# Kernel tuning notes

Measured on AMD Instinct MI355X. Metric: run time of the kernel, lower is better.

Reference implementation:

```python
import jax, jax.numpy as jnp
import numpy as np

N, E = 50000, 800000
HID, EDGE_DIM, HEADS = 128, 16, 4
C = HID // HEADS  # 32
NEG_SLOPE = 0.2  # GATv2Conv default negative_slope


def setup_inputs() -> dict:
    key = jax.random.key(0)
    ks = jax.random.split(key, 16)
    def glorot(k, shape):
        fan_in = shape[0]
        return jax.random.normal(k, shape, jnp.float32) / np.sqrt(fan_in)
    return {
        "x": jax.random.normal(ks[0], (N, HID), jnp.float32),
        "edge_index": jax.random.randint(ks[1], (2, E), 0, N, jnp.int64 if jax.config.jax_enable_x64 else jnp.int32),
        "edge_attr": jax.random.normal(ks[2], (E, EDGE_DIM), jnp.float32),
        # GATv2Conv params (lin_l, lin_r with bias; lin_edge bias-free; att; final bias)
        "Wl": glorot(ks[3], (HID, HID)),
        "bl": jnp.zeros((HID,), jnp.float32),
        "Wr": glorot(ks[4], (HID, HID)),
        "br": jnp.zeros((HID,), jnp.float32),
        "We": glorot(ks[5], (EDGE_DIM, HID)),
        "att": glorot(ks[6], (HEADS, C)),
        "bias_gat": jnp.zeros((HID,), jnp.float32),
        # RMSNorm weights
        "w_norm1": jnp.ones((HID,), jnp.float32),
        "w_norm2": jnp.ones((HID,), jnp.float32),
        # FFN params
        "ffn_w1": glorot(ks[7], (HID, 4 * HID)),
        "ffn_b1": jnp.zeros((4 * HID,), jnp.float32),
        "ffn_w2": glorot(ks[8], (4 * HID, HID)),
        "ffn_b2": jnp.zeros((HID,), jnp.float32),
    }


def rmsnorm(x, w):
    # torch.nn.RMSNorm with eps=None -> eps = finfo(dtype).eps
    eps = jnp.finfo(x.dtype).eps
    ms = jnp.mean(x * x, axis=-1, keepdims=True)
    return x * jax.lax.rsqrt(ms + eps) * w


def gatv2_conv(x, edge_index, edge_attr, Wl, bl, Wr, br, We, att, bias_gat):
    n = x.shape[0]
    h, c = att.shape
    xl = (x @ Wl + bl).reshape(n, h, c)   # source-side transform (x_j)
    xr = (x @ Wr + br).reshape(n, h, c)   # target-side transform (x_i)
    src, dst = edge_index[0], edge_index[1]
    e = (edge_attr @ We).reshape(-1, h, c)
    m = xl[src] + xr[dst] + e                       # [E, H, C] per-edge message pre-activation
    s = jnp.where(m > 0, m, NEG_SLOPE * m)          # LeakyReLU(0.2)
    logits = jnp.einsum('ehc,hc->eh', s, att)       # [E, H]
    # scatter-softmax over edges grouped by target node
    lmax = jax.ops.segment_max(logits, dst, num_segments=n)
    ex = jnp.exp(logits - lmax[dst])
    den = jax.ops.segment_sum(ex, dst, num_segments=n)
    alpha = ex / (den[dst] + 1e-16)                 # PyG softmax denominator guard
    out = jax.ops.segment_sum(alpha[..., None] * xl[src], dst, num_segments=n)
    return out.reshape(n, h * c) + bias_gat


def reference(x, edge_index, edge_attr, Wl, bl, Wr, br, We, att, bias_gat,
              w_norm1, w_norm2, ffn_w1, ffn_b1, ffn_w2, ffn_b2):
    x_attn = gatv2_conv(x, edge_index, edge_attr, Wl, bl, Wr, br, We, att, bias_gat)
    h = rmsnorm(x + x_attn, w_norm1)
    f = jax.nn.gelu(h @ ffn_w1 + ffn_b1, approximate=False) @ ffn_w2 + ffn_b2
    return rmsnorm(h + f, w_norm2)
```

## Files before the change

kernel.cpp:

```cpp
#include <hip/hip_runtime.h>

#define NN 50000
#define EE 800000

typedef unsigned short u16;

#define OFF_GAT  0u
#define OFF_XLB  6400000u
#define OFF_XRB  9600000u
#define OFF_SE   12800000u
#define OFF_CNT  14400000u
#define OFF_OFS  14450000u
#define OFF_H    6400000u
#define OFF_WLRT 14500004u
#define OFF_W1T  14516388u
#define OFF_W2T  14549156u

#define RMS_EPS 1.1920928955078125e-7f

typedef float f32x4v __attribute__((ext_vector_type(4)));
typedef short s16x8 __attribute__((ext_vector_type(8)));

__device__ __forceinline__ f32x4v mfma16(s16x8 a, s16x8 b, f32x4v c) {
  return __builtin_amdgcn_mfma_f32_16x16x32_bf16(a, b, c, 0, 0, 0);
}
__device__ __forceinline__ u16 f2b(float f) {
  unsigned int u = __float_as_uint(f);
  unsigned int r = (u + 0x7fffu + ((u >> 16) & 1u)) >> 16;
  return (u16)r;
}
__device__ __forceinline__ float b2f(u16 u) {
  union { float f; unsigned int i; } x; x.i = ((unsigned int)u) << 16; return x.f;
}
__device__ __forceinline__ s16x8 ld_bf16x8_f32(const float* __restrict__ p) {
  float4 v0 = *(const float4*)p;
  float4 v1 = *(const float4*)(p + 4);
  s16x8 r;
  r[0] = (short)f2b(v0.x); r[1] = (short)f2b(v0.y);
  r[2] = (short)f2b(v0.z); r[3] = (short)f2b(v0.w);
  r[4] = (short)f2b(v1.x); r[5] = (short)f2b(v1.y);
  r[6] = (short)f2b(v1.z); r[7] = (short)f2b(v1.w);
  return r;
}
__device__ __forceinline__ float readlane_f32(float v, int lane) {
  return __int_as_float(__builtin_amdgcn_readlane(__float_as_int(v), lane));
}
__device__ __forceinline__ int readlane_i32(int v, int lane) {
  return __builtin_amdgcn_readlane(v, lane);
}

__global__ __launch_bounds__(256) void k_prep(const float* __restrict__ Wl, const float* __restrict__ Wr,
    const float* __restrict__ W1, const float* __restrict__ W2,
    int* __restrict__ cnt, u16* __restrict__ wlrt, u16* __restrict__ w1t, u16* __restrict__ w2t)
{
  int i = blockIdx.x * 256 + threadIdx.x;
  if (i < NN) cnt[i] = 0;
  if (i < 32768) {
    int n = i >> 7, k = i & 127;
    float v = (n < 128) ? Wl[k * 128 + n] : Wr[k * 128 + (n - 128)];
    wlrt[i] = f2b(v);
  }
  {
    int n = i >> 7, k = i & 127;
    w1t[i] = f2b(W1[k * 512 + n]);
  }
  {
    int n = i >> 9, k = i & 511;
    w2t[i] = f2b(W2[k * 128 + n]);
  }
}

__global__ __launch_bounds__(256) void k_hist(const int* __restrict__ ei, int* __restrict__ cnt) {
  int e = blockIdx.x * 256 + threadIdx.x;
  if (e < EE) atomicAdd(&cnt[ei[EE + e]], 1);
}

__global__ __launch_bounds__(1024) void k_scan(const int* __restrict__ cnt,
    int* __restrict__ offs, int* __restrict__ pos)
{
  __shared__ int wsum[16];
  __shared__ int carry_s;
  int tid = threadIdx.x, lane = tid & 63, wv = tid >> 6;
  if (tid == 0) carry_s = 0;
  __syncthreads();
  for (int base = 0; base < NN; base += 1024) {
    int i = base + tid;
    int v = (i < NN) ? cnt[i] : 0;
    int x = v;
#pragma unroll
    for (int ofs = 1; ofs < 64; ofs <<= 1) {
      int y = __shfl_up(x, ofs);
      if (lane >= ofs) x += y;
    }
    if (lane == 63) wsum[wv] = x;
    __syncthreads();
    if (wv == 0) {
      int s = (lane < 16) ? wsum[lane] : 0;
#pragma unroll
      for (int ofs = 1; ofs < 16; ofs <<= 1) {
        int y = __shfl_up(s, ofs);
        if (lane >= ofs) s += y;
      }
      if (lane < 16) wsum[lane] = s;
    }
    __syncthreads();
    int wbase = (wv > 0) ? wsum[wv - 1] : 0;
    int incl = x + wbase + carry_s;
    if (i < NN) { offs[i + 1] = incl; pos[i] = incl - v; }
    if (base == 0 && tid == 0) offs[0] = 0;
    __syncthreads();
    if (tid == 1023) carry_s = incl;
    __syncthreads();
  }
}

__global__ __launch_bounds__(256) void k_permute(const int* __restrict__ ei,
    int* __restrict__ pos, int2* __restrict__ se)
{
  int e = blockIdx.x * 256 + threadIdx.x;
  if (e < EE) {
    int slot = atomicAdd(&pos[ei[EE + e]], 1);
    se[slot] = make_int2(ei[e], e);
  }
}

__global__ __launch_bounds__(256) void k1_mfma(const float* __restrict__ x, const u16* __restrict__ wlrt,
    const float* __restrict__ bl, const float* __restrict__ br,
    u16* __restrict__ xlb, u16* __restrict__ xrb)
{
  int tid = threadIdx.x;
  int w = tid >> 6, lane = tid & 63;
  int quad = lane >> 4, l16 = lane & 15;
  int row0 = blockIdx.x * 32;
  int ko = quad * 8;
  f32x4v acc[2][4];
#pragma unroll
  for (int mt = 0; mt < 2; ++mt)
#pragma unroll
    for (int nt = 0; nt < 4; ++nt) acc[mt][nt] = (f32x4v){0.f, 0.f, 0.f, 0.f};
#pragma unroll
  for (int ks = 0; ks < 4; ++ks) {
    int k0 = ks * 32 + ko;
    s16x8 a[2];
#pragma unroll
    for (int mt = 0; mt < 2; ++mt) {
      int row = row0 + mt * 16 + l16; if (row >= NN) row = NN - 1;
      a[mt] = ld_bf16x8_f32(x + row * 128 + k0);
    }
#pragma unroll
    for (int nt = 0; nt < 4; ++nt) {
      int col = w * 64 + nt * 16 + l16;
      s16x8 b = *(const s16x8*)(wlrt + col * 128 + k0);
      acc[0][nt] = mfma16(a[0], b, acc[0][nt]);
      acc[1][nt] = mfma16(a[1], b, acc[1][nt]);
    }
  }
#pragma unroll
  for (int nt = 0; nt < 4; ++nt) {
    int col = w * 64 + nt * 16 + l16;
    bool isl = col < 128;
    float bias = isl ? bl[col] : br[col - 128];
    u16* dst = isl ? xlb : xrb;
    int cc = isl ? col : col - 128;
#pragma unroll
    for (int mt = 0; mt < 2; ++mt)
#pragma unroll
      for (int r = 0; r < 4; ++r) {
        int row = row0 + mt * 16 + quad * 4 + r;
        if (row < NN) dst[row * 128 + cc] = f2b(acc[mt][nt][r] + bias);
      }
  }
}

__global__ __launch_bounds__(256) void k2_attn(
    const int* __restrict__ offs, const int2* __restrict__ se,
    const float* __restrict__ eattr,
    const float* __restrict__ att, const float* __restrict__ We,
    const u16* __restrict__ xlb, const u16* __restrict__ xrb,
    float* __restrict__ gat)
{
  int l = threadIdx.x & 63;
  int wid = (blockIdx.x * blockDim.x + threadIdx.x) >> 6;
  int nw = (gridDim.x * blockDim.x) >> 6;
  int c0 = 2 * l;
  const float2* We2 = (const float2*)We;
  float2 wef[16];
#pragma unroll
  for (int k = 0; k < 16; ++k) wef[k] = We2[k * 64 + l];
  float a0 = att[c0], a1 = att[c0 + 1];
  for (int d = wid; d < NN; d += nw) {
    int start = offs[d];
    int deg = offs[d + 1] - start;
    ushort2 xru = *(const ushort2*)(xrb + d * 128 + c0);
    float xr0 = b2f(xru.x), xr1 = b2f(xru.y);
    float mh = -1e30f, lh = 0.f, O0 = 0.f, O1 = 0.f;
    for (int base = 0; base < deg; base += 64) {
      bool act = (base + l) < deg;
      int idx = start + base + l;
      int2 sev = act ? se[idx] : make_int2(0, 0);
      int cnt = min(64, deg - base);
      for (int sub = 0; sub < cnt; sub += 4) {
        int eidq = __shfl(sev.y, sub + (l >> 4));
        float eav = eattr[eidq * 16 + (l & 15)];
        float p[4], xl0v[4], xl1v[4];
#pragma unroll
        for (int j2 = 0; j2 < 4; ++j2) {
          float ep0 = 0.f, ep1 = 0.f;
#pragma unroll
          for (int k = 0; k < 16; ++k) {
            float ek = readlane_f32(eav, j2 * 16 + k);
            ep0 = fmaf(ek, wef[k].x, ep0);
            ep1 = fmaf(ek, wef[k].y, ep1);
          }
          int sr = readlane_i32(sev.x, sub + j2);
          ushort2 xlu = *(const ushort2*)(xlb + sr * 128 + c0);
          float xl0 = b2f(xlu.x), xl1 = b2f(xlu.y);
          float m0 = xl0 + xr0 + ep0;
          float m1 = xl1 + xr1 + ep1;
          float s0 = m0 > 0.f ? m0 : 0.2f * m0;
          float s1 = m1 > 0.f ? m1 : 0.2f * m1;
          p[j2] = fmaf(s0, a0, s1 * a1);
          xl0v[j2] = xl0; xl1v[j2] = xl1;
        }
#pragma unroll
        for (int o = 1; o <= 8; o <<= 1) {
          p[0] += __shfl_xor(p[0], o);
          p[1] += __shfl_xor(p[1], o);
          p[2] += __shfl_xor(p[2], o);
          p[3] += __shfl_xor(p[3], o);
        }
#pragma unroll
        for (int j2 = 0; j2 < 4; ++j2) if (sub + j2 >= cnt) p[j2] = -1e30f;
        float nm = fmaxf(fmaxf(fmaxf(p[0], p[1]), fmaxf(p[2], p[3])), mh);
        float sc = __expf(mh - nm);
        float w0 = __expf(p[0] - nm), w1 = __expf(p[1] - nm);
        float w2 = __expf(p[2] - nm), w3 = __expf(p[3] - nm);
        lh = fmaf(lh, sc, (w0 + w1) + (w2 + w3));
        O0 = fmaf(O0, sc, fmaf(w0, xl0v[0], fmaf(w1, xl0v[1], fmaf(w2, xl0v[2], w3 * xl0v[3]))));
        O1 = fmaf(O1, sc, fmaf(w0, xl1v[0], fmaf(w1, xl1v[1], fmaf(w2, xl1v[2], w3 * xl1v[3]))));
        mh = nm;
      }
    }
    float inv = 1.f / (lh + 1e-16f);
    *(float2*)(gat + d * 128 + c0) = make_float2(O0 * inv, O1 * inv);
  }
}

__global__ __launch_bounds__(256) void k5_norm1(const float* __restrict__ x,
    const float* __restrict__ gat, const float* __restrict__ bg,
    const float* __restrict__ wn1, float* __restrict__ h)
{
  int l = threadIdx.x & 63;
  int row = blockIdx.x * 4 + (threadIdx.x >> 6);
  int c0 = 2 * l;
  float2 xu = *(const float2*)(x + row * 128 + c0);
  float2 gv = *(const float2*)(gat + row * 128 + c0);
  float2 bu = *(const float2*)(bg + c0);
  float v0 = xu.x + gv.x + bu.x;
  float v1 = xu.y + gv.y + bu.y;
  float ss = v0 * v0 + v1 * v1;
#pragma unroll
  for (int o = 1; o < 64; o <<= 1) ss += __shfl_xor(ss, o);
  float rr = rsqrtf(ss * (1.f / 128.f) + RMS_EPS);
  float2 wu = *(const float2*)(wn1 + c0);
  *(float2*)(h + row * 128 + c0) = make_float2(v0 * rr * wu.x, v1 * rr * wu.y);
}

__global__ __launch_bounds__(256) void k6_mfma(const float* __restrict__ h,
    const u16* __restrict__ w1t, const u16* __restrict__ w2t,
    const float* __restrict__ b1, const float* __restrict__ b2,
    const float* __restrict__ wn2, float* __restrict__ out)
{
  __shared__ u16 tls[32 * 520];
  __shared__ float red[4][32];
  int tid = threadIdx.x;
  int w = tid >> 6, lane = tid & 63;
  int quad = lane >> 4, l16 = lane & 15;
  int row0 = blockIdx.x * 32;
  int ko = quad * 8;

  f32x4v acc1[2][8];
#pragma unroll
  for (int mt = 0; mt < 2; ++mt)
#pragma unroll
    for (int nt = 0; nt < 8; ++nt) acc1[mt][nt] = (f32x4v){0.f, 0.f, 0.f, 0.f};
#pragma unroll
  for (int ks = 0; ks < 4; ++ks) {
    int k0 = ks * 32 + ko;
    s16x8 a[2];
#pragma unroll
    for (int mt = 0; mt < 2; ++mt) {
      int row = row0 + mt * 16 + l16; if (row >= NN) row = NN - 1;
      a[mt] = ld_bf16x8_f32(h + row * 128 + k0);
    }
#pragma unroll
    for (int nt = 0; nt < 8; ++nt) {
      int col = w * 128 + nt * 16 + l16;
      s16x8 b = *(const s16x8*)(w1t + col * 128 + k0);
      acc1[0][nt] = mfma16(a[0], b, acc1[0][nt]);
      acc1[1][nt] = mfma16(a[1], b, acc1[1][nt]);
    }
  }
#pragma unroll
  for (int nt = 0; nt < 8; ++nt) {
    int col = w * 128 + nt * 16 + l16;
    float bb = b1[col];
#pragma unroll
    for (int mt = 0; mt < 2; ++mt)
#pragma unroll
      for (int r = 0; r < 4; ++r) {
        float t = acc1[mt][nt][r] + bb;
        t = 0.5f * t * (1.f + erff(t * 0.70710678118654752f));
        tls[(mt * 16 + quad * 4 + r) * 520 + col] = f2b(t);
      }
  }
  __syncthreads();

  f32x4v acc2[2][2];
#pragma unroll
  for (int mt = 0; mt < 2; ++mt)
#pragma unroll
    for (int nt = 0; nt < 2; ++nt) acc2[mt][nt] = (f32x4v){0.f, 0.f, 0.f, 0.f};
#pragma unroll
  for (int ks = 0; ks < 16; ++ks) {
    int k0 = ks * 32 + ko;
    s16x8 a2[2];
#pragma unroll
    for (int mt = 0; mt < 2; ++mt)
      a2[mt] = *(const s16x8*)(tls + (mt * 16 + l16) * 520 + k0);
#pragma unroll
    for (int nt = 0; nt < 2; ++nt) {
      int col = w * 32 + nt * 16 + l16;
      s16x8 b = *(const s16x8*)(w2t + col * 512 + k0);
      acc2[0][nt] = mfma16(a2[0], b, acc2[0][nt]);
      acc2[1][nt] = mfma16(a2[1], b, acc2[1][nt]);
    }
  }
  int cols[2]; float bb2[2], wn[2];
#pragma unroll
  for (int nt = 0; nt < 2; ++nt) {
    cols[nt] = w * 32 + nt * 16 + l16;
    bb2[nt] = b2[cols[nt]];
    wn[nt] = wn2[cols[nt]];
  }
  float ov[2][2][4];
#pragma unroll
  for (int mt = 0; mt < 2; ++mt)
#pragma unroll
    for (int r = 0; r < 4; ++r) {
      int row = row0 + mt * 16 + quad * 4 + r;
      int rowc = row < NN ? row : NN - 1;
#pragma unroll
      for (int nt = 0; nt < 2; ++nt)
        ov[mt][nt][r] = h[rowc * 128 + cols[nt]] + acc2[mt][nt][r] + bb2[nt];
    }
#pragma unroll
  for (int mt = 0; mt < 2; ++mt)
#pragma unroll
    for (int r = 0; r < 4; ++r) {
      float q = ov[mt][0][r] * ov[mt][0][r] + ov[mt][1][r] * ov[mt][1][r];
      q += __shfl_xor(q, 1); q += __shfl_xor(q, 2);
      q += __shfl_xor(q, 4); q += __shfl_xor(q, 8);
      if (l16 == 0) red[w][mt * 16 + quad * 4 + r] = q;
    }
  __syncthreads();
#pragma unroll
  for (int mt = 0; mt < 2; ++mt)
#pragma unroll
    for (int r = 0; r < 4; ++r) {
      int rl = mt * 16 + quad * 4 + r;
      float tot = red[0][rl] + red[1][rl] + red[2][rl] + red[3][rl];
      float rr = rsqrtf(tot * (1.f / 128.f) + RMS_EPS);
      int row = row0 + rl;
      if (row < NN) {
        out[row * 128 + cols[0]] = ov[mt][0][r] * rr * wn[0];
        out[row * 128 + cols[1]] = ov[mt][1][r] * rr * wn[1];
      }
    }
}

extern "C" void kernel_launch(void* const* d_in, const int* in_sizes, int n_in,
                              void* d_out, int out_size, void* d_ws, size_t ws_size,
                              hipStream_t stream) {
  const float* x   = (const float*)d_in[0];
  const int*   ei  = (const int*)d_in[1];
  const float* ea  = (const float*)d_in[2];
  const float* Wl  = (const float*)d_in[3];
  const float* bl  = (const float*)d_in[4];
  const float* Wr  = (const float*)d_in[5];
  const float* br  = (const float*)d_in[6];
  const float* We  = (const float*)d_in[7];
  const float* att = (const float*)d_in[8];
  const float* bg  = (const float*)d_in[9];
  const float* wn1 = (const float*)d_in[10];
  const float* wn2 = (const float*)d_in[11];
  const float* W1  = (const float*)d_in[12];
  const float* b1  = (const float*)d_in[13];
  const float* W2  = (const float*)d_in[14];
  const float* b2  = (const float*)d_in[15];

  float* wsf = (float*)d_ws;
  int*   wsi = (int*)d_ws;

  float* gat  = wsf + OFF_GAT;
  u16* xlb    = (u16*)(wsf + OFF_XLB);
  u16* xrb    = (u16*)(wsf + OFF_XRB);
  int2* se    = (int2*)(wsf + OFF_SE);
  int* cnt    = wsi + OFF_CNT;
  int* pos    = wsi + OFF_CNT;
  int* offs   = wsi + OFF_OFS;
  float* hbuf = wsf + OFF_H;
  u16* wlrt   = (u16*)(wsf + OFF_WLRT);
  u16* w1t    = (u16*)(wsf + OFF_W1T);
  u16* w2t    = (u16*)(wsf + OFF_W2T);

  k_prep<<<256, 256, 0, stream>>>(Wl, Wr, W1, W2, cnt, wlrt, w1t, w2t);

  k_hist<<<(EE + 255) / 256, 256, 0, stream>>>(ei, cnt);
  k_scan<<<1, 1024, 0, stream>>>(cnt, offs, pos);
  k_permute<<<(EE + 255) / 256, 256, 0, stream>>>(ei, pos, se);

  k1_mfma<<<(NN + 31) / 32, 256, 0, stream>>>(x, wlrt, bl, br, xlb, xrb);

  k2_attn<<<2048, 256, 0, stream>>>(offs, se, ea, att, We, xlb, xrb, gat);

  k5_norm1<<<NN / 4, 256, 0, stream>>>(x, gat, bg, wn1, hbuf);

  k6_mfma<<<(NN + 31) / 32, 256, 0, stream>>>(hbuf, w1t, w2t, b1, b2, wn2, (float*)d_out);
}
```

Baseline: 546.8 us.

## Restructure FFN kernel: 512 threads, bf16 h copy, swizzled LDS, fast GELU

The FFN kernel now runs 8 waves per 32-row block, each owning fewer output columns. This lowers accumulator register pressure and raises parallelism. The norm1 kernel also writes a bf16 copy of h, so the first GEMM loads bf16 operands directly instead of converting fp32 per block. The padded LDS tile is replaced with an XOR-swizzled layout and reused for the reduction scratch. Exact erf GELU is replaced by a tanh-style sigmoid approximation, which changes numerics slightly relative to the exact-erf reference.

```diff
diff --git a/kernel.cpp b/kernel.cpp
--- a/kernel.cpp
+++ b/kernel.cpp
@@ -12,9 +12,10 @@
 #define OFF_CNT  14400000u
 #define OFF_OFS  14450000u
 #define OFF_H    6400000u
-#define OFF_WLRT 14500004u
-#define OFF_W1T  14516388u
-#define OFF_W2T  14549156u
+#define OFF_HB   12800000u
+#define OFF_WLRT 16000000u
+#define OFF_W1T  16016384u
+#define OFF_W2T  16049152u
 
 #define RMS_EPS 1.1920928955078125e-7f
 
@@ -47,6 +48,12 @@
 }
 __device__ __forceinline__ int readlane_i32(int v, int lane) {
   return __builtin_amdgcn_readlane(v, lane);
+}
+__device__ __forceinline__ float gelu_fast(float x) {
+  float x2 = x * x;
+  float y = x * fmaf(0.07135481283f, x2, 1.5957691216f);
+  float e = __expf(-y);
+  return x * __builtin_amdgcn_rcpf(1.0f + e);
 }
 
 __global__ __launch_bounds__(256) void k_prep(const float* __restrict__ Wl, const float* __restrict__ Wr,
@@ -248,7 +255,7 @@
 
 __global__ __launch_bounds__(256) void k5_norm1(const float* __restrict__ x,
     const float* __restrict__ gat, const float* __restrict__ bg,
-    const float* __restrict__ wn1, float* __restrict__ h)
+    const float* __restrict__ wn1, float* __restrict__ h, u16* __restrict__ hb)
 {
   int l = threadIdx.x & 63;
   int row = blockIdx.x * 4 + (threadIdx.x >> 6);
@@ -263,27 +270,36 @@
   for (int o = 1; o < 64; o <<= 1) ss += __shfl_xor(ss, o);
   float rr = rsqrtf(ss * (1.f / 128.f) + RMS_EPS);
   float2 wu = *(const float2*)(wn1 + c0);
-  *(float2*)(h + row * 128 + c0) = make_float2(v0 * rr * wu.x, v1 * rr * wu.y);
-}
-
-__global__ __launch_bounds__(256) void k6_mfma(const float* __restrict__ h,
+  float o0 = v0 * rr * wu.x, o1 = v1 * rr * wu.y;
+  *(float2*)(h + row * 128 + c0) = make_float2(o0, o1);
+  ushort2 hu; hu.x = f2b(o0); hu.y = f2b(o1);
+  *(ushort2*)(hb + row * 128 + c0) = hu;
+}
+
+__device__ __forceinline__ u16* tls_addr(u16* tls, int row, int col) {
+  int byte = (row << 10) + (col << 1);
+  byte ^= (row & 7) << 4;
+  return (u16*)((char*)tls + byte);
+}
+
+__global__ __launch_bounds__(512) void k6_mfma(const float* __restrict__ h,
+    const u16* __restrict__ hb,
     const u16* __restrict__ w1t, const u16* __restrict__ w2t,
     const float* __restrict__ b1, const float* __restrict__ b2,
     const float* __restrict__ wn2, float* __restrict__ out)
 {
-  __shared__ u16 tls[32 * 520];
-  __shared__ float red[4][32];
+  __shared__ u16 tls[32 * 512];
   int tid = threadIdx.x;
   int w = tid >> 6, lane = tid & 63;
   int quad = lane >> 4, l16 = lane & 15;
   int row0 = blockIdx.x * 32;
   int ko = quad * 8;
 
-  f32x4v acc1[2][8];
+  f32x4v acc1[2][4];
 #pragma unroll
   for (int mt = 0; mt < 2; ++mt)
 #pragma unroll
-    for (int nt = 0; nt < 8; ++nt) acc1[mt][nt] = (f32x4v){0.f, 0.f, 0.f, 0.f};
+    for (int nt = 0; nt < 4; ++nt) acc1[mt][nt] = (f32x4v){0.f, 0.f, 0.f, 0.f};
 #pragma unroll
   for (int ks = 0; ks < 4; ++ks) {
     int k0 = ks * 32 + ko;
@@ -291,74 +307,64 @@
 #pragma unroll
     for (int mt = 0; mt < 2; ++mt) {
       int row = row0 + mt * 16 + l16; if (row >= NN) row = NN - 1;
-      a[mt] = ld_bf16x8_f32(h + row * 128 + k0);
-    }
-#pragma unroll
-    for (int nt = 0; nt < 8; ++nt) {
-      int col = w * 128 + nt * 16 + l16;
+      a[mt] = *(const s16x8*)(hb + row * 128 + k0);
+    }
+#pragma unroll
+    for (int nt = 0; nt < 4; ++nt) {
+      int col = w * 64 + nt * 16 + l16;
       s16x8 b = *(const s16x8*)(w1t + col * 128 + k0);
       acc1[0][nt] = mfma16(a[0], b, acc1[0][nt]);
       acc1[1][nt] = mfma16(a[1], b, acc1[1][nt]);
     }
   }
 #pragma unroll
-  for (int nt = 0; nt < 8; ++nt) {
-    int col = w * 128 + nt * 16 + l16;
+  for (int nt = 0; nt < 4; ++nt) {
+    int col = w * 64 + nt * 16 + l16;
     float bb = b1[col];
 #pragma unroll
     for (int mt = 0; mt < 2; ++mt)
 #pragma unroll
       for (int r = 0; r < 4; ++r) {
-        float t = acc1[mt][nt][r] + bb;
-        t = 0.5f * t * (1.f + erff(t * 0.70710678118654752f));
-        tls[(mt * 16 + quad * 4 + r) * 520 + col] = f2b(t);
+        float t = gelu_fast(acc1[mt][nt][r] + bb);
+        *tls_addr(tls, mt * 16 + quad * 4 + r, col) = f2b(t);
       }
   }
   __syncthreads();
 
-  f32x4v acc2[2][2];
-#pragma unroll
-  for (int mt = 0; mt < 2; ++mt)
-#pragma unroll
-    for (int nt = 0; nt < 2; ++nt) acc2[mt][nt] = (f32x4v){0.f, 0.f, 0.f, 0.f};
+  f32x4v acc2[2];
+  acc2[0] = (f32x4v){0.f, 0.f, 0.f, 0.f};
+  acc2[1] = (f32x4v){0.f, 0.f, 0.f, 0.f};
+  int col = w * 16 + l16;
+  const u16* bptr = w2t + col * 512;
 #pragma unroll
   for (int ks = 0; ks < 16; ++ks) {
     int k0 = ks * 32 + ko;
     s16x8 a2[2];
 #pragma unroll
     for (int mt = 0; mt < 2; ++mt)
-      a2[mt] = *(const s16x8*)(tls + (mt * 16 + l16) * 520 + k0);
-#pragma unroll
-    for (int nt = 0; nt < 2; ++nt) {
-      int col = w * 32 + nt * 16 + l16;
-      s16x8 b = *(const s16x8*)(w2t + col * 512 + k0);
-      acc2[0][nt] = mfma16(a2[0], b, acc2[0][nt]);
-      acc2[1][nt] = mfma16(a2[1], b, acc2[1][nt]);
-    }
-  }
-  int cols[2]; float bb2[2], wn[2];
-#pragma unroll
-  for (int nt = 0; nt < 2; ++nt) {
-    cols[nt] = w * 32 + nt * 16 + l16;
-    bb2[nt] = b2[cols[nt]];
-    wn[nt] = wn2[cols[nt]];
-  }
-  float ov[2][2][4];
+      a2[mt] = *(const s16x8*)tls_addr(tls, mt * 16 + l16, k0);
+    s16x8 b = *(const s16x8*)(bptr + k0);
+    acc2[0] = mfma16(a2[0], b, acc2[0]);
+    acc2[1] = mfma16(a2[1], b, acc2[1]);
+  }
+
+  float bb2 = b2[col], wn = wn2[col];
+  float ov[2][4];
 #pragma unroll
   for (int mt = 0; mt < 2; ++mt)
 #pragma unroll
     for (int r = 0; r < 4; ++r) {
       int row = row0 + mt * 16 + quad * 4 + r;
       int rowc = row < NN ? row : NN - 1;
-#pragma unroll
-      for (int nt = 0; nt < 2; ++nt)
-        ov[mt][nt][r] = h[rowc * 128 + cols[nt]] + acc2[mt][nt][r] + bb2[nt];
-    }
+      ov[mt][r] = h[rowc * 128 + col] + acc2[mt][r] + bb2;
+    }
+  __syncthreads();
+  float (*red)[32] = (float (*)[32])(void*)tls;
 #pragma unroll
   for (int mt = 0; mt < 2; ++mt)
 #pragma unroll
     for (int r = 0; r < 4; ++r) {
-      float q = ov[mt][0][r] * ov[mt][0][r] + ov[mt][1][r] * ov[mt][1][r];
+      float q = ov[mt][r] * ov[mt][r];
       q += __shfl_xor(q, 1); q += __shfl_xor(q, 2);
       q += __shfl_xor(q, 4); q += __shfl_xor(q, 8);
       if (l16 == 0) red[w][mt * 16 + quad * 4 + r] = q;
@@ -369,13 +375,11 @@
 #pragma unroll
     for (int r = 0; r < 4; ++r) {
       int rl = mt * 16 + quad * 4 + r;
-      float tot = red[0][rl] + red[1][rl] + red[2][rl] + red[3][rl];
+      float tot = ((red[0][rl] + red[1][rl]) + (red[2][rl] + red[3][rl]))
+                + ((red[4][rl] + red[5][rl]) + (red[6][rl] + red[7][rl]));
       float rr = rsqrtf(tot * (1.f / 128.f) + RMS_EPS);
       int row = row0 + rl;
-      if (row < NN) {
-        out[row * 128 + cols[0]] = ov[mt][0][r] * rr * wn[0];
-        out[row * 128 + cols[1]] = ov[mt][1][r] * rr * wn[1];
-      }
+      if (row < NN) out[row * 128 + col] = ov[mt][r] * rr * wn;
     }
 }
 
@@ -410,6 +414,7 @@
   int* pos    = wsi + OFF_CNT;
   int* offs   = wsi + OFF_OFS;
   float* hbuf = wsf + OFF_H;
+  u16* hb     = (u16*)(wsf + OFF_HB);
   u16* wlrt   = (u16*)(wsf + OFF_WLRT);
   u16* w1t    = (u16*)(wsf + OFF_W1T);
   u16* w2t    = (u16*)(wsf + OFF_W2T);
@@ -424,7 +429,7 @@
 
   k2_attn<<<2048, 256, 0, stream>>>(offs, se, ea, att, We, xlb, xrb, gat);
 
-  k5_norm1<<<NN / 4, 256, 0, stream>>>(x, gat, bg, wn1, hbuf);
-
-  k6_mfma<<<(NN + 31) / 32, 256, 0, stream>>>(hbuf, w1t, w2t, b1, b2, wn2, (float*)d_out);
-}
+  k5_norm1<<<NN / 4, 256, 0, stream>>>(x, gat, bg, wn1, hbuf, hb);
+
+  k6_mfma<<<(NN + 31) / 32, 512, 0, stream>>>(hbuf, hb, w1t, w2t, b1, b2, wn2, (float*)d_out);
+}
```

Measured after the change: 514.8 us. 1.06x faster.
